# Kernel optimization log

Hardware: AMD Instinct MI355X
Metric: run time of the kernel (lower is better)

## Reference

```python
import jax, jax.numpy as jnp
import numpy as np

N_NODES = 50000
N_EDGES = 800000
N_FEAT = 128
HIDDEN = 128
N_CLASSES = 10
N_LAYERS = 3
N_GRAPHS = 512


def setup_inputs() -> dict:
    key = jax.random.key(0)
    ks = jax.random.split(key, 16)
    s = 1.0 / np.sqrt(HIDDEN)
    inp = {
        "x": jax.random.normal(ks[0], (N_NODES, N_FEAT), jnp.float32),
        "edge_index": jax.random.randint(ks[1], (2, N_EDGES), 0, N_NODES, jnp.int64),
        "batch": jnp.sort(jax.random.randint(ks[2], (N_NODES,), 0, N_GRAPHS, jnp.int64)),
        "num_graphs": N_GRAPHS,
        "conv1_wl": jax.random.normal(ks[3], (N_FEAT, HIDDEN), jnp.float32) * s,
        "conv1_wr": jax.random.normal(ks[4], (N_FEAT, HIDDEN), jnp.float32) * s,
        "conv1_b": jnp.zeros((HIDDEN,), jnp.float32),
        "convs_wl": jax.random.normal(ks[5], (N_LAYERS - 1, HIDDEN, HIDDEN), jnp.float32) * s,
        "convs_wr": jax.random.normal(ks[6], (N_LAYERS - 1, HIDDEN, HIDDEN), jnp.float32) * s,
        "convs_b": jnp.zeros((N_LAYERS - 1, HIDDEN), jnp.float32),
        "gate_w": jax.random.normal(ks[7], (HIDDEN, 1), jnp.float32) * s,
        "gate_b": jnp.zeros((1,), jnp.float32),
        "lin1_w": jax.random.normal(ks[8], (HIDDEN, HIDDEN), jnp.float32) * s,
        "lin1_b": jnp.zeros((HIDDEN,), jnp.float32),
        "lin2_w": jax.random.normal(ks[9], (HIDDEN, N_CLASSES), jnp.float32) * s,
        "lin2_b": jnp.zeros((N_CLASSES,), jnp.float32),
    }
    return inp


def _sage_conv(x, src, dst, inv_deg, wl, wr, b):
    # mean aggregation of source-node features at destination nodes
    agg = jax.ops.segment_sum(x[src], dst, num_segments=N_NODES)  # [N, d]
    agg = agg * inv_deg
    return agg @ wl + x @ wr + b


def _global_attention(x, batch, num_graphs, gate_w, gate_b):
    gate = (x @ gate_w + gate_b)[:, 0]                      # [N]
    m = jax.ops.segment_max(gate, batch, num_segments=num_graphs)
    m = jnp.where(jnp.isfinite(m), m, 0.0)
    g = jnp.exp(gate - m[batch])                            # stable segment softmax
    den = jax.ops.segment_sum(g, batch, num_segments=num_graphs)
    attn = g / den[batch]
    return jax.ops.segment_sum(attn[:, None] * x, batch, num_segments=num_graphs)


def reference(x, edge_index, batch, num_graphs,
              conv1_wl, conv1_wr, conv1_b,
              convs_wl, convs_wr, convs_b,
              gate_w, gate_b, lin1_w, lin1_b, lin2_w, lin2_b):
    src, dst = edge_index[0], edge_index[1]
    deg = jax.ops.segment_sum(jnp.ones((src.shape[0],), x.dtype), dst,
                              num_segments=N_NODES)
    inv_deg = (1.0 / jnp.maximum(deg, 1.0))[:, None]

    h = jax.nn.relu(_sage_conv(x, src, dst, inv_deg, conv1_wl, conv1_wr, conv1_b))
    for i in range(convs_wl.shape[0]):
        h = jax.nn.relu(_sage_conv(h, src, dst, inv_deg,
                                   convs_wl[i], convs_wr[i], convs_b[i]))

    pooled = _global_attention(h, batch, num_graphs, gate_w, gate_b)  # [G, H]
    out = jax.nn.relu(pooled @ lin1_w + lin1_b)
    # dropout p=0.5 is identity at eval time
    logits = out @ lin2_w + lin2_b
    return jax.nn.log_softmax(logits, axis=-1)
```

## Files before the change

kernel.cpp:

```cpp
#include <hip/hip_runtime.h>
#include <math.h>

#define N_NODES 50000
#define N_PAD   50048
#define N_EDGES 800000
#define FEAT 128
#define K2 256
#define N_GRAPHS 512
#define N_CLASSES 10
#define BCAP 64
#define BROW 264
#define OROW 72
#define AGG_BLOCKS 2048

typedef __attribute__((ext_vector_type(8))) short short8;
typedef __attribute__((ext_vector_type(4))) float floatx4;

__device__ __forceinline__ float bflo(unsigned u) { return __uint_as_float(u << 16); }
__device__ __forceinline__ float bfhi(unsigned u) { return __uint_as_float(u & 0xffff0000u); }
__device__ __forceinline__ unsigned short f2bf(float f) {
    unsigned u = __float_as_uint(f);
    u = (u + 0x7fffu + ((u >> 16) & 1u)) >> 16;
    return (unsigned short)u;
}
__device__ __forceinline__ unsigned pack2(float a, float b) {
    return (unsigned)f2bf(a) | ((unsigned)f2bf(b) << 16);
}

__global__ __launch_bounds__(256) void fill_bucket(
    const int* __restrict__ src, const int* __restrict__ dst,
    int* __restrict__ cnt, unsigned short* __restrict__ bucket) {
    int e = blockIdx.x * 256 + threadIdx.x;
    int d = dst[e];
    int p = atomicAdd(&cnt[d], 1);
    if (p < BCAP) bucket[(size_t)d * BCAP + p] = (unsigned short)src[e];
}

__global__ __launch_bounds__(256) void setup_kernel(
    const float* __restrict__ x, unsigned short* __restrict__ A,
    const float* __restrict__ wl1, const float* __restrict__ wr1,
    const float* __restrict__ wl23, const float* __restrict__ wr23,
    unsigned short* __restrict__ wt,
    const int* __restrict__ batch, int* __restrict__ goffs) {
    int b = blockIdx.x;
    if (b < 6250) {
        int idx = b * 256 + threadIdx.x;
        if (idx < N_NODES * 32) {
            int n = idx >> 5, f4 = idx & 31;
            float4 v = ((const float4*)(x + (size_t)n * FEAT))[f4];
            uint2 o = make_uint2(pack2(v.x, v.y), pack2(v.z, v.w));
            *(uint2*)(A + (size_t)n * K2 + FEAT + f4 * 4) = o;
        }
    } else if (b < 6250 + 384) {
        int idx = (b - 6250) * 256 + threadIdx.x;
        int layer = idx >> 15;
        int r = idx & 32767;
        int n = r >> 8, k = r & 255;
        const float* wl = (layer == 0) ? wl1 : wl23 + (size_t)(layer - 1) * FEAT * FEAT;
        const float* wr = (layer == 0) ? wr1 : wr23 + (size_t)(layer - 1) * FEAT * FEAT;
        float v = (k < FEAT) ? wl[k * FEAT + n] : wr[(k - FEAT) * FEAT + n];
        wt[idx] = f2bf(v);
    } else {
        int g = (b - 6250 - 384) * 256 + threadIdx.x;
        if (g > N_GRAPHS) return;
        int lo = 0, hi = N_NODES;
        while (lo < hi) {
            int mid = (lo + hi) >> 1;
            if (batch[mid] < g) lo = mid + 1; else hi = mid;
        }
        goffs[g] = lo;
    }
}

__device__ __forceinline__ void acc8(float* acc, uint4 u) {
    acc[0] += bflo(u.x); acc[1] += bfhi(u.x);
    acc[2] += bflo(u.y); acc[3] += bfhi(u.y);
    acc[4] += bflo(u.z); acc[5] += bfhi(u.z);
    acc[6] += bflo(u.w); acc[7] += bfhi(u.w);
}

__global__ __launch_bounds__(256) void aggregate_bf16(
    const unsigned short* __restrict__ hin, const int* __restrict__ cnt,
    const unsigned short* __restrict__ bucket, unsigned short* __restrict__ aggout) {
    int lane = threadIdx.x & 63;
    int g = lane >> 4;
    int l16 = lane & 15;
    int wid = (blockIdx.x << 2) + (threadIdx.x >> 6);
    const int nw = gridDim.x << 2;

    int n = wid;
    if (n >= N_NODES) return;
    int deg = cnt[n];

    while (true) {
        const unsigned short* cp = bucket + (size_t)n * BCAP;
        int c = min(deg, BCAP);
        int nq = c >> 2;
        int rem = c & 3;

        int nn = n + nw;
        int dnext = 0;
        if (nn < N_NODES) {
            dnext = cnt[nn];
            unsigned short bpre = bucket[(size_t)nn * BCAP + lane];
            asm volatile("" :: "v"((int)bpre));
        }

        float acc[8];
        #pragma unroll
        for (int i = 0; i < 8; ++i) acc[i] = 0.f;

        int i = 0;
        for (; i + 4 <= nq; i += 4) {
            int s0 = cp[i * 4 + g];
            int s1 = cp[i * 4 + 4 + g];
            int s2 = cp[i * 4 + 8 + g];
            int s3 = cp[i * 4 + 12 + g];
            uint4 u0 = *(const uint4*)(hin + (size_t)s0 * K2 + l16 * 8);
            uint4 u1 = *(const uint4*)(hin + (size_t)s1 * K2 + l16 * 8);
            uint4 u2 = *(const uint4*)(hin + (size_t)s2 * K2 + l16 * 8);
            uint4 u3 = *(const uint4*)(hin + (size_t)s3 * K2 + l16 * 8);
            acc8(acc, u0); acc8(acc, u1); acc8(acc, u2); acc8(acc, u3);
        }
        if (i + 2 <= nq) {
            int s0 = cp[i * 4 + g];
            int s1 = cp[i * 4 + 4 + g];
            uint4 u0 = *(const uint4*)(hin + (size_t)s0 * K2 + l16 * 8);
            uint4 u1 = *(const uint4*)(hin + (size_t)s1 * K2 + l16 * 8);
            acc8(acc, u0); acc8(acc, u1);
            i += 2;
        }
        if (i < nq) {
            int s0 = cp[i * 4 + g];
            uint4 u0 = *(const uint4*)(hin + (size_t)s0 * K2 + l16 * 8);
            acc8(acc, u0);
        }
        if (g < rem) {
            int s0 = cp[nq * 4 + g];
            uint4 u0 = *(const uint4*)(hin + (size_t)s0 * K2 + l16 * 8);
            acc8(acc, u0);
        }
        #pragma unroll
        for (int j = 0; j < 8; ++j) {
            acc[j] += __shfl_xor(acc[j], 16);
            acc[j] += __shfl_xor(acc[j], 32);
        }
        if (g == 0) {
            float inv = 1.0f / fmaxf((float)deg, 1.0f);
            uint4 o;
            o.x = pack2(acc[0] * inv, acc[1] * inv);
            o.y = pack2(acc[2] * inv, acc[3] * inv);
            o.z = pack2(acc[4] * inv, acc[5] * inv);
            o.w = pack2(acc[6] * inv, acc[7] * inv);
            *(uint4*)(aggout + (size_t)n * K2 + l16 * 8) = o;
        }
        if (nn >= N_NODES) break;
        n = nn;
        deg = dnext;
    }
}

__global__ __launch_bounds__(256) void gemm_mfma(
    const unsigned short* __restrict__ Ain, unsigned short* __restrict__ Aout,
    const unsigned short* __restrict__ Wt, const float* __restrict__ bias,
    const float* __restrict__ gate_w, float* __restrict__ gate) {
    __shared__ unsigned short sB[64 * BROW];
    __shared__ unsigned short sOut[4][32 * OROW];
    int t = threadIdx.x;
    int wave = t >> 6, lane = t & 63;
    int q = lane >> 4, l16 = lane & 15;

    const int nwg_q = 97, nwg_r = 6;
    int orig = blockIdx.x;
    int xcd = orig & 7, idx = orig >> 3;
    int wgid = (xcd < nwg_r) ? xcd * (nwg_q + 1) + idx
                             : nwg_r * (nwg_q + 1) + (xcd - nwg_r) * nwg_q + idx;
    int tileM = wgid >> 1;
    int nh = wgid & 1;
    int row0 = tileM * 128 + wave * 32;

    const unsigned short* pa0 = Ain + (size_t)(row0 + l16) * K2 + q * 8;
    const unsigned short* pa1 = pa0 + 16 * K2;
    short8 a0[8], a1[8];
    #pragma unroll
    for (int ks = 0; ks < 8; ++ks) {
        a0[ks] = *(const short8*)(pa0 + ks * 32);
        a1[ks] = *(const short8*)(pa1 + ks * 32);
    }

    #pragma unroll
    for (int i = 0; i < 8; ++i) {
        int flat = i * 256 + t;
        int rw = flat >> 5, fr = flat & 31;
        uint4 v = *((const uint4*)(Wt + (size_t)(nh * 64 + rw) * K2) + fr);
        *(uint4*)(&sB[rw * BROW + fr * 8]) = v;
    }
    __syncthreads();

    floatx4 acc[2][4];
    #pragma unroll
    for (int i = 0; i < 2; ++i)
        #pragma unroll
        for (int j = 0; j < 4; ++j) acc[i][j] = (floatx4){0.f, 0.f, 0.f, 0.f};

    #pragma unroll
    for (int ks = 0; ks < 8; ++ks) {
        #pragma unroll
        for (int nb = 0; nb < 4; ++nb) {
            short8 b = *(const short8*)(&sB[(nb * 16 + l16) * BROW + ks * 32 + q * 8]);
            acc[0][nb] = __builtin_amdgcn_mfma_f32_16x16x32_bf16(a0[ks], b, acc[0][nb], 0, 0, 0);
            acc[1][nb] = __builtin_amdgcn_mfma_f32_16x16x32_bf16(a1[ks], b, acc[1][nb], 0, 0, 0);
        }
    }

    float bv[4], gwv[4];
    #pragma unroll
    for (int nb = 0; nb < 4; ++nb) bv[nb] = bias[nh * 64 + nb * 16 + l16];
    if (gate_w) {
        #pragma unroll
        for (int nb = 0; nb < 4; ++nb) gwv[nb] = gate_w[nh * 64 + nb * 16 + l16];
    }

    #pragma unroll
    for (int band = 0; band < 2; ++band) {
        #pragma unroll
        for (int r = 0; r < 4; ++r) {
            int lr = band * 16 + q * 4 + r;
            float gsum = 0.f;
            #pragma unroll
            for (int nb = 0; nb < 4; ++nb) {
                float v = fmaxf(acc[band][nb][r] + bv[nb], 0.f);
                sOut[wave][lr * OROW + nb * 16 + l16] = f2bf(v);
                if (gate_w) gsum += v * gwv[nb];
            }
            if (gate_w) {
                gsum += __shfl_xor(gsum, 1);
                gsum += __shfl_xor(gsum, 2);
                gsum += __shfl_xor(gsum, 4);
                gsum += __shfl_xor(gsum, 8);
                int m = row0 + lr;
                if (l16 == 0 && m < N_NODES) atomicAdd(&gate[m], gsum);
            }
        }
    }

    int r2 = lane >> 1, h2 = lane & 1;
    size_t gbase = (size_t)(row0 + r2) * K2 + FEAT + nh * 64 + h2 * 32;
    #pragma unroll
    for (int j = 0; j < 2; ++j) {
        uint4 v0 = *(uint4*)(&sOut[wave][r2 * OROW + h2 * 32 + j * 16]);
        uint4 v1 = *(uint4*)(&sOut[wave][r2 * OROW + h2 * 32 + j * 16 + 8]);
        *(uint4*)(Aout + gbase + j * 16) = v0;
        *(uint4*)(Aout + gbase + j * 16 + 8) = v1;
    }
}

__global__ __launch_bounds__(256) void pool_head(
    const unsigned short* __restrict__ h, const float* __restrict__ gate,
    const int* __restrict__ goffs,
    const float* __restrict__ w1, const float* __restrict__ b1,
    const float* __restrict__ w2, const float* __restrict__ b2,
    float* __restrict__ out) {
    __shared__ float sred[4];
    __shared__ float facc[4][128];
    __shared__ float pv[128], qv[128], lg[N_CLASSES];
    int g = blockIdx.x;
    int s = goffs[g], e = goffs[g + 1];
    int t = threadIdx.x;
    int wave = t >> 6, lane = t & 63;

    if (s < e) {
        float mx = -INFINITY;
        for (int n = s + t; n < e; n += 256) mx = fmaxf(mx, gate[n]);
        #pragma unroll
        for (int off = 32; off; off >>= 1) mx = fmaxf(mx, __shfl_xor(mx, off));
        if (lane == 0) sred[wave] = mx;
        __syncthreads();
        float m = fmaxf(fmaxf(sred[0], sred[1]), fmaxf(sred[2], sred[3]));
        __syncthreads();
        float d = 0.f;
        for (int n = s + t; n < e; n += 256) d += __expf(gate[n] - m);
        #pragma unroll
        for (int off = 32; off; off >>= 1) d += __shfl_xor(d, off);
        if (lane == 0) sred[wave] = d;
        __syncthreads();
        float den = sred[0] + sred[1] + sred[2] + sred[3];
        float acc0 = 0.f, acc1 = 0.f;
        for (int n = s + wave; n < e; n += 4) {
            float gn = __expf(gate[n] - m);
            unsigned u = *(const unsigned*)(h + (size_t)n * K2 + lane * 2);
            acc0 += gn * bflo(u);
            acc1 += gn * bfhi(u);
        }
        facc[wave][lane * 2]     = acc0;
        facc[wave][lane * 2 + 1] = acc1;
        __syncthreads();
        if (t < 128) pv[t] = (facc[0][t] + facc[1][t] + facc[2][t] + facc[3][t]) / den;
    } else {
        if (t < 128) pv[t] = 0.f;
    }
    __syncthreads();

    if (t < 128) {
        float acc = b1[t];
        #pragma unroll 4
        for (int k = 0; k < 128; ++k) acc += pv[k] * w1[k * FEAT + t];
        qv[t] = fmaxf(acc, 0.f);
    }
    __syncthreads();
    if (t < N_CLASSES) {
        float a = b2[t];
        #pragma unroll 4
        for (int k = 0; k < 128; ++k) a += qv[k] * w2[k * N_CLASSES + t];
        lg[t] = a;
    }
    __syncthreads();
    if (t < N_CLASSES) {
        float m = -INFINITY;
        #pragma unroll
        for (int j = 0; j < N_CLASSES; ++j) m = fmaxf(m, lg[j]);
        float sum = 0.f;
        #pragma unroll
        for (int j = 0; j < N_CLASSES; ++j) sum += __expf(lg[j] - m);
        out[(size_t)g * N_CLASSES + t] = lg[t] - m - __logf(sum);
    }
}

static inline size_t align256(size_t x) { return (x + 255) & ~(size_t)255; }

extern "C" void kernel_launch(void* const* d_in, const int* in_sizes, int n_in,
                              void* d_out, int out_size, void* d_ws, size_t ws_size,
                              hipStream_t stream) {
    const float* x        = (const float*)d_in[0];
    const int*   ei       = (const int*)d_in[1];
    const int*   batch    = (const int*)d_in[2];
    const float* conv1_wl = (const float*)d_in[4];
    const float* conv1_wr = (const float*)d_in[5];
    const float* conv1_b  = (const float*)d_in[6];
    const float* convs_wl = (const float*)d_in[7];
    const float* convs_wr = (const float*)d_in[8];
    const float* convs_b  = (const float*)d_in[9];
    const float* gate_w   = (const float*)d_in[10];
    const float* lin1_w   = (const float*)d_in[12];
    const float* lin1_b   = (const float*)d_in[13];
    const float* lin2_w   = (const float*)d_in[14];
    const float* lin2_b   = (const float*)d_in[15];
    float* out = (float*)d_out;

    const int* src = ei;
    const int* dst = ei + N_EDGES;

    char* w = (char*)d_ws;
    size_t off = 0;
    unsigned short* A0   = (unsigned short*)(w + off); off += align256((size_t)N_PAD * K2 * 2);
    unsigned short* A1   = (unsigned short*)(w + off); off += align256((size_t)N_PAD * K2 * 2);
    unsigned short* bkt  = (unsigned short*)(w + off); off += align256((size_t)N_NODES * BCAP * 2);
    unsigned short* wt   = (unsigned short*)(w + off); off += align256((size_t)3 * FEAT * K2 * 2);
    int*   i_goff = (int*)(w + off);   off += align256((size_t)(N_GRAPHS + 1) * 4);
    char* zbase = w + off;
    int*   i_cnt  = (int*)(w + off);   off += align256((size_t)N_NODES * 4);
    float* f_gate = (float*)(w + off); off += align256((size_t)N_NODES * 4);
    size_t zbytes = (size_t)((w + off) - zbase);

    hipMemsetAsync(zbase, 0, zbytes, stream);

    fill_bucket<<<N_EDGES / 256, 256, 0, stream>>>(src, dst, i_cnt, bkt);
    setup_kernel<<<6250 + 384 + 3, 256, 0, stream>>>(
        x, A0, conv1_wl, conv1_wr, convs_wl, convs_wr, wt, batch, i_goff);

    const int GB = (N_PAD / 128) * 2;

    aggregate_bf16<<<AGG_BLOCKS, 256, 0, stream>>>(A0 + FEAT, i_cnt, bkt, A0);
    gemm_mfma<<<GB, 256, 0, stream>>>(A0, A1, wt, conv1_b, nullptr, nullptr);
    aggregate_bf16<<<AGG_BLOCKS, 256, 0, stream>>>(A1 + FEAT, i_cnt, bkt, A1);
    gemm_mfma<<<GB, 256, 0, stream>>>(A1, A0, wt + FEAT * K2, convs_b, nullptr, nullptr);
    aggregate_bf16<<<AGG_BLOCKS, 256, 0, stream>>>(A0 + FEAT, i_cnt, bkt, A0);
    gemm_mfma<<<GB, 256, 0, stream>>>(A0, A1, wt + 2 * FEAT * K2, convs_b + FEAT,
                                      gate_w, f_gate);

    pool_head<<<N_GRAPHS, 256, 0, stream>>>(A1 + FEAT, f_gate, i_goff,
                                            lin1_w, lin1_b, lin2_w, lin2_b, out);
}
```

Measured before the change: 305.2 us.

## Fuse bucket fill into setup kernel with range-partitioned, padded atomic counters

After: 291.7 us. 1.05x faster.

```diff
diff --git a/kernel.cpp b/kernel.cpp
--- a/kernel.cpp
+++ b/kernel.cpp
@@ -13,6 +13,12 @@
 #define OROW 72
 #define AGG_BLOCKS 2048
 
+#define FILL_BLOCKS 1000
+#define FILL_ITER 25
+#define RANGE_NODES 6250
+#define CNT_STRIDE 16
+#define PREP_BLOCKS (FILL_BLOCKS + 6250 + 384 + 3)
+
 typedef __attribute__((ext_vector_type(8))) short short8;
 typedef __attribute__((ext_vector_type(4))) float floatx4;
 
@@ -27,32 +33,37 @@
     return (unsigned)f2bf(a) | ((unsigned)f2bf(b) << 16);
 }
 
-__global__ __launch_bounds__(256) void fill_bucket(
+__global__ __launch_bounds__(256) void prep_kernel(
     const int* __restrict__ src, const int* __restrict__ dst,
-    int* __restrict__ cnt, unsigned short* __restrict__ bucket) {
-    int e = blockIdx.x * 256 + threadIdx.x;
-    int d = dst[e];
-    int p = atomicAdd(&cnt[d], 1);
-    if (p < BCAP) bucket[(size_t)d * BCAP + p] = (unsigned short)src[e];
-}
-
-__global__ __launch_bounds__(256) void setup_kernel(
+    int* __restrict__ cnt, unsigned short* __restrict__ bucket,
     const float* __restrict__ x, unsigned short* __restrict__ A,
     const float* __restrict__ wl1, const float* __restrict__ wr1,
     const float* __restrict__ wl23, const float* __restrict__ wr23,
     unsigned short* __restrict__ wt,
     const int* __restrict__ batch, int* __restrict__ goffs) {
-    int b = blockIdx.x;
-    if (b < 6250) {
-        int idx = b * 256 + threadIdx.x;
+    int b = blockIdx.x, t = threadIdx.x;
+    if (b < FILL_BLOCKS) {
+        int chunk = b >> 3, r = b & 7;
+        int lo = r * RANGE_NODES, hi = lo + RANGE_NODES;
+        int base = chunk * (FILL_ITER * 256) + t;
+        for (int i = 0; i < FILL_ITER; ++i) {
+            int e = base + i * 256;
+            int d = dst[e];
+            if (d >= lo && d < hi) {
+                int p = atomicAdd(&cnt[d << 4], 1);
+                if (p < BCAP) bucket[(size_t)d * BCAP + p] = (unsigned short)src[e];
+            }
+        }
+    } else if (b < FILL_BLOCKS + 6250) {
+        int idx = (b - FILL_BLOCKS) * 256 + t;
         if (idx < N_NODES * 32) {
             int n = idx >> 5, f4 = idx & 31;
             float4 v = ((const float4*)(x + (size_t)n * FEAT))[f4];
             uint2 o = make_uint2(pack2(v.x, v.y), pack2(v.z, v.w));
             *(uint2*)(A + (size_t)n * K2 + FEAT + f4 * 4) = o;
         }
-    } else if (b < 6250 + 384) {
-        int idx = (b - 6250) * 256 + threadIdx.x;
+    } else if (b < FILL_BLOCKS + 6250 + 384) {
+        int idx = (b - FILL_BLOCKS - 6250) * 256 + t;
         int layer = idx >> 15;
         int r = idx & 32767;
         int n = r >> 8, k = r & 255;
@@ -61,7 +72,7 @@
         float v = (k < FEAT) ? wl[k * FEAT + n] : wr[(k - FEAT) * FEAT + n];
         wt[idx] = f2bf(v);
     } else {
-        int g = (b - 6250 - 384) * 256 + threadIdx.x;
+        int g = (b - FILL_BLOCKS - 6250 - 384) * 256 + t;
         if (g > N_GRAPHS) return;
         int lo = 0, hi = N_NODES;
         while (lo < hi) {
@@ -90,7 +101,7 @@
 
     int n = wid;
     if (n >= N_NODES) return;
-    int deg = cnt[n];
+    int deg = cnt[n << 4];
 
     while (true) {
         const unsigned short* cp = bucket + (size_t)n * BCAP;
@@ -101,7 +112,7 @@
         int nn = n + nw;
         int dnext = 0;
         if (nn < N_NODES) {
-            dnext = cnt[nn];
+            dnext = cnt[nn << 4];
             unsigned short bpre = bucket[(size_t)nn * BCAP + lane];
             asm volatile("" :: "v"((int)bpre));
         }
@@ -358,14 +369,14 @@
     unsigned short* wt   = (unsigned short*)(w + off); off += align256((size_t)3 * FEAT * K2 * 2);
     int*   i_goff = (int*)(w + off);   off += align256((size_t)(N_GRAPHS + 1) * 4);
     char* zbase = w + off;
-    int*   i_cnt  = (int*)(w + off);   off += align256((size_t)N_NODES * 4);
+    int*   i_cnt  = (int*)(w + off);   off += align256((size_t)N_NODES * CNT_STRIDE * 4);
     float* f_gate = (float*)(w + off); off += align256((size_t)N_NODES * 4);
     size_t zbytes = (size_t)((w + off) - zbase);
 
     hipMemsetAsync(zbase, 0, zbytes, stream);
 
-    fill_bucket<<<N_EDGES / 256, 256, 0, stream>>>(src, dst, i_cnt, bkt);
-    setup_kernel<<<6250 + 384 + 3, 256, 0, stream>>>(
+    prep_kernel<<<PREP_BLOCKS, 256, 0, stream>>>(
+        src, dst, i_cnt, bkt,
         x, A0, conv1_wl, conv1_wr, convs_wl, convs_wr, wt, batch, i_goff);
 
     const int GB = (N_PAD / 128) * 2;
```
